# Performance work log

Hardware: AMD Instinct MI355X
Metric: run time of the kernel (lower is better)

Reference implementation:

```python
import jax, jax.numpy as jnp
import numpy as np

EPS_NORM = 1e-12   # F.normalize eps
EPS_MERGE = 1e-8   # weighted-average denominator eps


def setup_inputs() -> dict:
    key = jax.random.key(0)
    k1, k2, k3 = jax.random.split(key, 3)
    B, S, D, G = 4, 4096, 768, 64
    x = jax.random.normal(k1, (B, S, D), dtype=jnp.float32)
    source = jax.random.uniform(k2, (B, S, S), dtype=jnp.float32)
    position_ids = jnp.arange(B * S, dtype=jnp.int32).reshape(B, S)
    Wg = jax.random.normal(k3, (D, G), dtype=jnp.float32) / np.sqrt(D)
    return {"x": x, "source": source, "position_ids": position_ids,
            "Wg": Wg, "r": 4, "window_size": 16}


def _select_pairs(sim, r):
    """Greedy non-overlapping adjacent-pair selection.
    sim: (B, nw, W-1) adjacent cosine sims. Returns bool (B, nw, W-1):
    selected edges (exactly r per window when r <= min maximal matching)."""
    B, nw, E = sim.shape
    W = E + 1
    order = jnp.argsort(-sim, axis=-1)            # descending similarity
    tok = jnp.arange(W)
    edge = jnp.arange(E)

    def step(carry, idx):
        mask, cnt, sel = carry                    # mask:(B,nw,W) cnt:(B,nw) sel:(B,nw,E)
        mi = jnp.take_along_axis(mask, idx[..., None], axis=-1)[..., 0]
        mj = jnp.take_along_axis(mask, idx[..., None] + 1, axis=-1)[..., 0]
        take = (~mi) & (~mj) & (cnt < r)
        hit = (tok == idx[..., None]) | (tok == idx[..., None] + 1)
        mask = mask | (take[..., None] & hit)
        sel = sel | (take[..., None] & (edge == idx[..., None]))
        cnt = cnt + take.astype(jnp.int32)
        return (mask, cnt, sel), None

    init = (jnp.zeros((B, nw, W), bool), jnp.zeros((B, nw), jnp.int32),
            jnp.zeros((B, nw, E), bool))
    (_, _, sel), _ = jax.lax.scan(step, init, jnp.moveaxis(order, -1, 0))
    return sel


def reference(x, source, position_ids, Wg, r, window_size):
    B, S, D = x.shape
    W = window_size
    nw = S // W                                   # S % W == 0 by construction
    N = source.shape[-1]
    xw = x.reshape(B, nw, W, D)
    sw = source.reshape(B, nw, W, N)
    pw = position_ids.reshape(B, nw, W)

    g = jnp.einsum('bnwd,dg->bnwg', xw, Wg)       # grouping embedding
    norms = jnp.linalg.norm(g, axis=-1)           # (B,nw,W)
    gn = g / jnp.maximum(norms[..., None], EPS_NORM)
    sim = jnp.sum(gn[..., :-1, :] * gn[..., 1:, :], axis=-1)  # (B,nw,W-1)

    sel = _select_pairs(sim, r)                   # (B,nw,W-1), exactly r True per window

    # weighted average of each adjacent pair by grouping-embedding norms
    wi, wj = norms[..., :-1], norms[..., 1:]
    tot = wi + wj + EPS_MERGE
    mx = (wi[..., None] * xw[..., :-1, :] + wj[..., None] * xw[..., 1:, :]) / tot[..., None]
    ms = sw[..., :-1, :] + sw[..., 1:, :]

    selL = jnp.pad(sel, ((0, 0), (0, 0), (0, 1)))          # token k is left of a merged pair
    mx_full = jnp.concatenate([mx, xw[..., -1:, :]], axis=-2)
    ms_full = jnp.concatenate([ms, sw[..., -1:, :]], axis=-2)
    y_x = jnp.where(selL[..., None], mx_full, xw)
    y_s = jnp.where(selL[..., None], ms_full, sw)

    # drop the right token of every merged pair; keep order (stable argsort)
    rmask = jnp.pad(sel, ((0, 0), (0, 0), (1, 0)))          # token k is right of a merged pair
    perm = jnp.argsort(rmask, axis=-1, stable=True)[..., :W - r]  # (B,nw,W-r)

    x_out = jnp.take_along_axis(y_x, perm[..., None], axis=-2).reshape(B, nw * (W - r), D)
    s_out = jnp.take_along_axis(y_s, perm[..., None], axis=-2).reshape(B, nw * (W - r), N)
    p_out = jnp.take_along_axis(pw, perm, axis=-1).reshape(B, nw * (W - r))
    return x_out, s_out, p_out
```

## Files before the change

kernel.cpp:

```cpp
#include <hip/hip_runtime.h>
#include <math.h>

namespace {
constexpr int Bc = 4, Sc = 4096, Dc = 768, Gc = 64, Wc = 16, Rc = 4;
constexpr int NWc = Sc / Wc;
constexpr int KEEPc = Wc - Rc;
constexpr int Ec = Wc - 1;
constexpr int NQc = Dc / 4;
constexpr int PQ = NQc + 1;
constexpr size_t X_ELEMS = (size_t)Bc * NWc * KEEPc * Dc;
constexpr size_t S_ELEMS = (size_t)Bc * NWc * KEEPc * Sc;
constexpr int NROWS = Bc * NWc * KEEPc;

typedef float vf4 __attribute__((ext_vector_type(4)));
typedef float f32x4 __attribute__((ext_vector_type(4)));
typedef short bf16x8 __attribute__((ext_vector_type(8)));

__device__ inline short f2bf(float f) {
  return __builtin_bit_cast(short, (__bf16)f);
}
}

__global__ __launch_bounds__(256)
void tm_select(const float* __restrict__ x, const int* __restrict__ pos,
               const float* __restrict__ Wg, float* __restrict__ out,
               int* __restrict__ meta) {
  const int wid = blockIdx.x;
  const int b = wid >> 8;
  const int n = wid & (NWc - 1);
  const int tid = threadIdx.x;
  const int lane = tid & 63;
  const int wq = tid >> 6;

  __shared__ float4 xs4[Wc * PQ];
  __shared__ float gl[Wc][Gc];

  const size_t winTok = (size_t)(b * Sc + n * Wc);
  const float4* xg = reinterpret_cast<const float4*>(x + winTok * Dc);

#pragma unroll
  for (int i = 0; i < 12; ++i) {
    const int idx = tid + 256 * i;
    const int r = idx / NQc;
    const int c = idx - r * NQc;
    xs4[r * PQ + c] = xg[idx];
  }
  __syncthreads();

  const int arow = lane & 15;
  const int kg = lane >> 4;
  const int col = 16 * wq + arow;
  f32x4 cacc = {0.f, 0.f, 0.f, 0.f};

  for (int s = 0; s < 24; ++s) {
    const float4 a0 = xs4[arow * PQ + s * 8 + kg * 2];
    const float4 a1 = xs4[arow * PQ + s * 8 + kg * 2 + 1];
    bf16x8 af;
    af[0] = f2bf(a0.x); af[1] = f2bf(a0.y); af[2] = f2bf(a0.z); af[3] = f2bf(a0.w);
    af[4] = f2bf(a1.x); af[5] = f2bf(a1.y); af[6] = f2bf(a1.z); af[7] = f2bf(a1.w);
    const int kbase = s * 32 + kg * 8;
    bf16x8 bf;
#pragma unroll
    for (int j = 0; j < 8; ++j) bf[j] = f2bf(Wg[(size_t)(kbase + j) * Gc + col]);
    cacc = __builtin_amdgcn_mfma_f32_16x16x32_bf16(af, bf, cacc, 0, 0, 0);
  }

#pragma unroll
  for (int r = 0; r < 4; ++r) gl[kg * 4 + r][col] = cacc[r];
  __syncthreads();

  float red[Wc + Ec];
  {
    float g[Wc];
#pragma unroll
    for (int w = 0; w < Wc; ++w) g[w] = gl[w][lane];
#pragma unroll
    for (int w = 0; w < Wc; ++w) red[w] = g[w] * g[w];
#pragma unroll
    for (int e = 0; e < Ec; ++e) red[Wc + e] = g[e] * g[e + 1];
  }
#pragma unroll
  for (int m = 1; m < 64; m <<= 1) {
#pragma unroll
    for (int i = 0; i < Wc + Ec; ++i) red[i] += __shfl_xor(red[i], m, 64);
  }

  float nr[Wc];
#pragma unroll
  for (int w = 0; w < Wc; ++w) nr[w] = sqrtf(red[w]);

  float sv[Ec];
#pragma unroll
  for (int e = 0; e < Ec; ++e)
    sv[e] = red[Wc + e] / (fmaxf(nr[e], 1e-12f) * fmaxf(nr[e + 1], 1e-12f));

  unsigned sel = 0, used = 0;
#pragma unroll
  for (int round = 0; round < Rc; ++round) {
    float best = -1e30f;
    int bi = 0;
#pragma unroll
    for (int e = 0; e < Ec; ++e) {
      const bool ok = ((used >> e) & 3u) == 0u;
      const float v = ok ? sv[e] : -1e30f;
      if (v > best) { best = v; bi = e; }
    }
    sel |= (1u << bi);
    used |= (3u << bi);
  }

#pragma unroll
  for (int j3 = 0; j3 < 3; ++j3) {
    const int k = wq * 3 + j3;
    int w = 0, c = 0;
#pragma unroll
    for (int t = 0; t < Wc; ++t) {
      const bool kept = (t == 0) || (((sel >> (t - 1)) & 1u) == 0u);
      if (kept && c == k) w = t;
      c += kept ? 1 : 0;
    }
    const bool mg = (w < Ec) && (((sel >> w) & 1u) != 0u);
    float wi = 0.f, wj = 0.f;
#pragma unroll
    for (int t = 0; t < Wc; ++t) {
      wi = (t == w) ? nr[t] : wi;
      wj = (t == (w + 1)) ? nr[t] : wj;
    }
    float aS = 1.f, bS = 0.f;
    if (mg) {
      const float tot = wi + wj + 1e-8f;
      aS = wi / tot;
      bS = wj / tot;
    }
    const float4* r1 = &xs4[w * PQ];
    const float4* r2 = &xs4[(mg ? (w + 1) : w) * PQ];
    vf4* o = reinterpret_cast<vf4*>(out + (size_t)(wid * KEEPc + k) * Dc);
#pragma unroll
    for (int it = 0; it < 3; ++it) {
      const int i = lane + 64 * it;
      const float4 a = r1[i];
      const float4 bb = r2[i];
      vf4 rr;
      rr.x = fmaf(aS, a.x, bS * bb.x);
      rr.y = fmaf(aS, a.y, bS * bb.y);
      rr.z = fmaf(aS, a.z, bS * bb.z);
      rr.w = fmaf(aS, a.w, bS * bb.w);
      __builtin_nontemporal_store(rr, o + i);
    }
  }

  if (wq == 0 && lane < KEEPc) {
    const int k = lane;
    int w = 0, c = 0;
#pragma unroll
    for (int t = 0; t < Wc; ++t) {
      const bool kept = (t == 0) || (((sel >> (t - 1)) & 1u) == 0u);
      if (kept && c == k) w = t;
      c += kept ? 1 : 0;
    }
    const bool mg = (w < Ec) && (((sel >> w) & 1u) != 0u);
    const int row = wid * KEEPc + k;
    meta[row] = w | (mg ? 16 : 0);
    out[X_ELEMS + S_ELEMS + (size_t)row] = (float)pos[winTok + w];
  }
}

__global__ __launch_bounds__(1024)
void tm_srows(const float* __restrict__ src, const int* __restrict__ meta,
              float* __restrict__ outs) {
  const int gid = blockIdx.x;
  const int t = threadIdx.x;

  const int mt = meta[gid];
  const int w = mt & 15;
  const bool mg = (mt & 16) != 0;

  const int b = gid / (NWc * KEEPc);
  const int m = gid - b * (NWc * KEEPc);
  const int n = m / KEEPc;

  const vf4* s1 = reinterpret_cast<const vf4*>(src + (size_t)(b * Sc + n * Wc + w) * Sc);
  vf4 a = s1[t];
  if (mg) a = a + s1[t + (Sc / 4)];
  __builtin_nontemporal_store(a, reinterpret_cast<vf4*>(outs + (size_t)gid * Sc) + t);
}

extern "C" void kernel_launch(void* const* d_in, const int* in_sizes, int n_in,
                              void* d_out, int out_size, void* d_ws, size_t ws_size,
                              hipStream_t stream) {
  const float* x = (const float*)d_in[0];
  const float* src = (const float*)d_in[1];
  const int* pos = (const int*)d_in[2];
  const float* Wg = (const float*)d_in[3];
  float* out = (float*)d_out;
  int* meta = (int*)d_ws;

  tm_select<<<dim3(Bc * NWc), dim3(256), 0, stream>>>(x, pos, Wg, out, meta);
  tm_srows<<<dim3(NROWS), dim3(1024), 0, stream>>>(src, meta, out + X_ELEMS);
}
```

Measured before the change: 117.7 us.

## Fuse selection and source-row gather into one kernel, drop x shared staging

```diff
diff --git a/kernel.cpp b/kernel.cpp
--- a/kernel.cpp
+++ b/kernel.cpp
@@ -7,10 +7,9 @@
 constexpr int KEEPc = Wc - Rc;
 constexpr int Ec = Wc - 1;
 constexpr int NQc = Dc / 4;
-constexpr int PQ = NQc + 1;
+constexpr int SQ4 = Sc / 4;
 constexpr size_t X_ELEMS = (size_t)Bc * NWc * KEEPc * Dc;
 constexpr size_t S_ELEMS = (size_t)Bc * NWc * KEEPc * Sc;
-constexpr int NROWS = Bc * NWc * KEEPc;
 
 typedef float vf4 __attribute__((ext_vector_type(4)));
 typedef float f32x4 __attribute__((ext_vector_type(4)));
@@ -21,52 +20,42 @@
 }
 }
 
-__global__ __launch_bounds__(256)
-void tm_select(const float* __restrict__ x, const int* __restrict__ pos,
-               const float* __restrict__ Wg, float* __restrict__ out,
-               int* __restrict__ meta) {
+__global__ __launch_bounds__(512)
+void tm_fused(const float* __restrict__ x, const float* __restrict__ src,
+              const int* __restrict__ pos, const float* __restrict__ Wg,
+              float* __restrict__ out) {
   const int wid = blockIdx.x;
   const int b = wid >> 8;
   const int n = wid & (NWc - 1);
   const int tid = threadIdx.x;
   const int lane = tid & 63;
-  const int wq = tid >> 6;
+  const int wv = tid >> 6;
 
-  __shared__ float4 xs4[Wc * PQ];
   __shared__ float gl[Wc][Gc];
 
   const size_t winTok = (size_t)(b * Sc + n * Wc);
   const float4* xg = reinterpret_cast<const float4*>(x + winTok * Dc);
 
+  if (wv < 4) {
+    const int arow = lane & 15;
+    const int kg = lane >> 4;
+    const int col = 16 * wv + arow;
+    f32x4 cacc = {0.f, 0.f, 0.f, 0.f};
+    for (int s = 0; s < 24; ++s) {
+      const float4 a0 = xg[arow * NQc + s * 8 + kg * 2];
+      const float4 a1 = xg[arow * NQc + s * 8 + kg * 2 + 1];
+      bf16x8 af;
+      af[0] = f2bf(a0.x); af[1] = f2bf(a0.y); af[2] = f2bf(a0.z); af[3] = f2bf(a0.w);
+      af[4] = f2bf(a1.x); af[5] = f2bf(a1.y); af[6] = f2bf(a1.z); af[7] = f2bf(a1.w);
+      const int kbase = s * 32 + kg * 8;
+      bf16x8 bf;
 #pragma unroll
-  for (int i = 0; i < 12; ++i) {
-    const int idx = tid + 256 * i;
-    const int r = idx / NQc;
-    const int c = idx - r * NQc;
-    xs4[r * PQ + c] = xg[idx];
+      for (int j = 0; j < 8; ++j) bf[j] = f2bf(Wg[(size_t)(kbase + j) * Gc + col]);
+      cacc = __builtin_amdgcn_mfma_f32_16x16x32_bf16(af, bf, cacc, 0, 0, 0);
+    }
+#pragma unroll
+    for (int r = 0; r < 4; ++r) gl[kg * 4 + r][col] = cacc[r];
   }
-  __syncthreads();
-
-  const int arow = lane & 15;
-  const int kg = lane >> 4;
-  const int col = 16 * wq + arow;
-  f32x4 cacc = {0.f, 0.f, 0.f, 0.f};
-
-  for (int s = 0; s < 24; ++s) {
-    const float4 a0 = xs4[arow * PQ + s * 8 + kg * 2];
-    const float4 a1 = xs4[arow * PQ + s * 8 + kg * 2 + 1];
-    bf16x8 af;
-    af[0] = f2bf(a0.x); af[1] = f2bf(a0.y); af[2] = f2bf(a0.z); af[3] = f2bf(a0.w);
-    af[4] = f2bf(a1.x); af[5] = f2bf(a1.y); af[6] = f2bf(a1.z); af[7] = f2bf(a1.w);
-    const int kbase = s * 32 + kg * 8;
-    bf16x8 bf;
-#pragma unroll
-    for (int j = 0; j < 8; ++j) bf[j] = f2bf(Wg[(size_t)(kbase + j) * Gc + col]);
-    cacc = __builtin_amdgcn_mfma_f32_16x16x32_bf16(af, bf, cacc, 0, 0, 0);
-  }
-
-#pragma unroll
-  for (int r = 0; r < 4; ++r) gl[kg * 4 + r][col] = cacc[r];
   __syncthreads();
 
   float red[Wc + Ec];
@@ -96,7 +85,7 @@
 
   unsigned sel = 0, used = 0;
 #pragma unroll
-  for (int round = 0; round < Rc; ++round) {
+  for (int r = 0; r < Rc; ++r) {
     float best = -1e30f;
     int bi = 0;
 #pragma unroll
@@ -109,80 +98,83 @@
     used |= (3u << bi);
   }
 
-#pragma unroll
-  for (int j3 = 0; j3 < 3; ++j3) {
-    const int k = wq * 3 + j3;
-    int w = 0, c = 0;
+  unsigned long long wmap = 0ull;
+  unsigned mgb = 0;
+  {
+    int c = 0;
 #pragma unroll
     for (int t = 0; t < Wc; ++t) {
       const bool kept = (t == 0) || (((sel >> (t - 1)) & 1u) == 0u);
-      if (kept && c == k) w = t;
-      c += kept ? 1 : 0;
+      if (kept) {
+        wmap |= (unsigned long long)t << (4 * c);
+        if (t < Ec && ((sel >> t) & 1u)) mgb |= 1u << c;
+        ++c;
+      }
     }
-    const bool mg = (w < Ec) && (((sel >> w) & 1u) != 0u);
-    float wi = 0.f, wj = 0.f;
+  }
+
+  const vf4* src4 = reinterpret_cast<const vf4*>(src);
+  vf4* outS4 = reinterpret_cast<vf4*>(out + X_ELEMS);
+#pragma unroll 1
+  for (int j = 0; j < 24; j += 4) {
+    vf4 v[4];
+    int kk[4], part[4];
 #pragma unroll
-    for (int t = 0; t < Wc; ++t) {
-      wi = (t == w) ? nr[t] : wi;
-      wj = (t == (w + 1)) ? nr[t] : wj;
+    for (int jj = 0; jj < 4; ++jj) {
+      const int ch = wv + 8 * (j + jj);
+      kk[jj] = ch >> 4;
+      part[jj] = ch & 15;
+      const int wrow = (int)((wmap >> (4 * kk[jj])) & 15ull);
+      v[jj] = src4[(winTok + wrow) * SQ4 + part[jj] * 64 + lane];
     }
+#pragma unroll
+    for (int jj = 0; jj < 4; ++jj) {
+      if ((mgb >> kk[jj]) & 1u) {
+        const int wrow = (int)((wmap >> (4 * kk[jj])) & 15ull);
+        v[jj] = v[jj] + src4[(winTok + wrow + 1) * SQ4 + part[jj] * 64 + lane];
+      }
+    }
+#pragma unroll
+    for (int jj = 0; jj < 4; ++jj) {
+      __builtin_nontemporal_store(
+          v[jj], outS4 + ((size_t)wid * KEEPc + kk[jj]) * SQ4 + part[jj] * 64 + lane);
+    }
+  }
+
+  const vf4* xg4 = reinterpret_cast<const vf4*>(x + winTok * Dc);
+#pragma unroll 1
+  for (int k = wv; k < KEEPc; k += 8) {
+    const int w = (int)((wmap >> (4 * k)) & 15ull);
+    const bool mg = ((mgb >> k) & 1u) != 0;
     float aS = 1.f, bS = 0.f;
     if (mg) {
-      const float tot = wi + wj + 1e-8f;
-      aS = wi / tot;
-      bS = wj / tot;
+      float wi_ = 0.f, wj_ = 0.f;
+#pragma unroll
+      for (int t2 = 0; t2 < Wc; ++t2) {
+        wi_ = (t2 == w) ? nr[t2] : wi_;
+        wj_ = (t2 == w + 1) ? nr[t2] : wj_;
+      }
+      const float tot = wi_ + wj_ + 1e-8f;
+      aS = wi_ / tot;
+      bS = wj_ / tot;
     }
-    const float4* r1 = &xs4[w * PQ];
-    const float4* r2 = &xs4[(mg ? (w + 1) : w) * PQ];
+    const vf4* r1 = xg4 + (size_t)w * NQc;
+    const vf4* r2 = xg4 + (size_t)(mg ? (w + 1) : w) * NQc;
     vf4* o = reinterpret_cast<vf4*>(out + (size_t)(wid * KEEPc + k) * Dc);
 #pragma unroll
     for (int it = 0; it < 3; ++it) {
       const int i = lane + 64 * it;
-      const float4 a = r1[i];
-      const float4 bb = r2[i];
-      vf4 rr;
-      rr.x = fmaf(aS, a.x, bS * bb.x);
-      rr.y = fmaf(aS, a.y, bS * bb.y);
-      rr.z = fmaf(aS, a.z, bS * bb.z);
-      rr.w = fmaf(aS, a.w, bS * bb.w);
-      __builtin_nontemporal_store(rr, o + i);
+      const vf4 a = r1[i];
+      const vf4 bb = r2[i];
+      __builtin_nontemporal_store(aS * a + bS * bb, o + i);
     }
   }
 
-  if (wq == 0 && lane < KEEPc) {
-    const int k = lane;
-    int w = 0, c = 0;
-#pragma unroll
-    for (int t = 0; t < Wc; ++t) {
-      const bool kept = (t == 0) || (((sel >> (t - 1)) & 1u) == 0u);
-      if (kept && c == k) w = t;
-      c += kept ? 1 : 0;
-    }
-    const bool mg = (w < Ec) && (((sel >> w) & 1u) != 0u);
-    const int row = wid * KEEPc + k;
-    meta[row] = w | (mg ? 16 : 0);
-    out[X_ELEMS + S_ELEMS + (size_t)row] = (float)pos[winTok + w];
+  if (wv == 0 && lane < KEEPc) {
+    const int w = (int)((wmap >> (4 * lane)) & 15ull);
+    out[X_ELEMS + S_ELEMS + (size_t)(wid * KEEPc + lane)] =
+        (float)pos[winTok + w];
   }
-}
-
-__global__ __launch_bounds__(1024)
-void tm_srows(const float* __restrict__ src, const int* __restrict__ meta,
-              float* __restrict__ outs) {
-  const int gid = blockIdx.x;
-  const int t = threadIdx.x;
-
-  const int mt = meta[gid];
-  const int w = mt & 15;
-  const bool mg = (mt & 16) != 0;
-
-  const int b = gid / (NWc * KEEPc);
-  const int m = gid - b * (NWc * KEEPc);
-  const int n = m / KEEPc;
-
-  const vf4* s1 = reinterpret_cast<const vf4*>(src + (size_t)(b * Sc + n * Wc + w) * Sc);
-  vf4 a = s1[t];
-  if (mg) a = a + s1[t + (Sc / 4)];
-  __builtin_nontemporal_store(a, reinterpret_cast<vf4*>(outs + (size_t)gid * Sc) + t);
 }
 
 extern "C" void kernel_launch(void* const* d_in, const int* in_sizes, int n_in,
@@ -193,8 +185,6 @@
   const int* pos = (const int*)d_in[2];
   const float* Wg = (const float*)d_in[3];
   float* out = (float*)d_out;
-  int* meta = (int*)d_ws;
 
-  tm_select<<<dim3(Bc * NWc), dim3(256), 0, stream>>>(x, pos, Wg, out, meta);
-  tm_srows<<<dim3(NROWS), dim3(1024), 0, stream>>>(src, meta, out + X_ELEMS);
+  tm_fused<<<dim3(Bc * NWc), dim3(512), 0, stream>>>(x, src, pos, Wg, out);
 }
```

After: 132.8 us. 1.13x slower.
